# Kernel optimization log

Hardware: AMD Instinct MI355X
Metric: run time of the kernel (lower is better)

## Reference

```python
import jax, jax.numpy as jnp
import numpy as np

D_MODEL = 1024
B, T = 4, 2048
LN_EPS = 1e-5


def setup_inputs() -> dict:
    key = jax.random.key(0)
    ks = jax.random.split(key, 8)
    d = D_MODEL
    x = jax.random.normal(ks[0], (B, T, d), dtype=jnp.float32)
    # linear params (fan-in scaled)
    W_in = jax.random.normal(ks[1], (d, 4 * d), dtype=jnp.float32) / np.sqrt(d)
    b_in = jnp.zeros((4 * d,), dtype=jnp.float32)
    W_out = jax.random.normal(ks[2], (2 * d, d), dtype=jnp.float32) / np.sqrt(2 * d)
    b_out = jnp.zeros((d,), dtype=jnp.float32)
    # LRU initializer (matches the torch module's initializer())
    rng = np.random.default_rng(0)
    r_min, r_max = 0.9, 0.999
    u1 = rng.random(d)
    u2 = rng.random(d)
    nu_log = np.log(-0.5 * np.log(u1 * (r_max ** 2 - r_min ** 2) + r_min ** 2))
    theta_log = np.log(u2 * np.pi * 2)
    gamma_log = np.log(np.sqrt(1 - np.exp(-np.exp(nu_log)) ** 2))
    # LayerNorm affine params
    ln_w = jnp.ones((2 * d,), dtype=jnp.float32)
    ln_b = jnp.zeros((2 * d,), dtype=jnp.float32)
    return {
        "x": x,
        "W_in": W_in, "b_in": b_in,
        "nu_log": jnp.asarray(nu_log, dtype=jnp.float32),
        "theta_log": jnp.asarray(theta_log, dtype=jnp.float32),
        "gamma_log": jnp.asarray(gamma_log, dtype=jnp.float32),
        "ln_w": ln_w, "ln_b": ln_b,
        "W_out": W_out, "b_out": b_out,
    }


def _complex_scan(in_r, in_i, f_r, f_i):
    """h_t = f * h_{t-1} + in_t over axis=1, complex math in real/imag pairs."""
    def combine(l, r):
        a1r, a1i, b1r, b1i = l
        a2r, a2i, b2r, b2i = r
        ar = a2r * a1r - a2i * a1i
        ai = a2r * a1i + a2i * a1r
        br = a2r * b1r - a2i * b1i + b2r
        bi = a2r * b1i + a2i * b1r + b2i
        return (ar, ai, br, bi)
    fr = jnp.broadcast_to(f_r, in_r.shape)
    fi = jnp.broadcast_to(f_i, in_i.shape)
    _, _, hr, hi = jax.lax.associative_scan(combine, (fr, fi, in_r, in_i), axis=1)
    return hr, hi


def reference(x, W_in, b_in, nu_log, theta_log, gamma_log, ln_w, ln_b, W_out, b_out):
    d = x.shape[-1]
    u = x @ W_in + b_in                       # [B, T, 4d]
    v, o = u[..., :2 * d], u[..., 2 * d:]     # each [B, T, 2d]
    nu = jnp.exp(-jnp.exp(nu_log))            # [d]
    theta = jnp.exp(theta_log)
    gamma = jnpp_exp = jnp.exp(gamma_log)
    f_r = nu * jnp.cos(theta)
    f_i = nu * jnp.sin(theta)
    in_r = gamma * v[..., :d]                 # [B, T, d]
    in_i = gamma * v[..., d:]
    h_r, h_i = _complex_scan(in_r, in_i, f_r, f_i)
    y = jnp.concatenate([h_r, h_i], axis=-1) * jax.nn.silu(o)  # [B, T, 2d]
    mu = jnp.mean(y, axis=-1, keepdims=True)
    var = jnp.mean(jnp.square(y - mu), axis=-1, keepdims=True)
    y = (y - mu) * jax.lax.rsqrt(var + LN_EPS) * ln_w + ln_b
    return y @ W_out + b_out                  # [B, T, d]
```

## Files before the change

### kernel.cpp

```cpp
#include <hip/hip_runtime.h>
#include <hip/hip_bf16.h>

#define D_MODEL 1024
#define BB 4
#define TT 2048
#define ROWS (BB*TT)
#define NCHUNK 32
#define CHLEN 64

typedef __attribute__((ext_vector_type(8))) short short8;
typedef __attribute__((ext_vector_type(4))) float floatx4;

static __device__ __forceinline__ ushort f2bf(float f) {
    union { float f; unsigned u; } v; v.f = f;
    unsigned r = v.u + 0x7FFF + ((v.u >> 16) & 1);
    return (ushort)(r >> 16);
}
static __device__ __forceinline__ float bf2f(ushort b) {
    union { unsigned u; float f; } v; v.u = ((unsigned)b) << 16;
    return v.f;
}

#define GLOAD_LDS16(gp, lp)                                                 \
    __builtin_amdgcn_global_load_lds(                                       \
        (const __attribute__((address_space(1))) void*)(gp),                \
        (__attribute__((address_space(3))) void*)(lp), 16, 0, 0)

#define PREP_A 8192
#define PREP_B 4096
#define PREP_C 2048
__global__ __launch_bounds__(256) void prep_all(
    const float* __restrict__ x, ushort* __restrict__ xb,
    const float* __restrict__ W_in, ushort* __restrict__ WinT,
    const float* __restrict__ W_out, ushort* __restrict__ W1T,
    const float* __restrict__ lnw, const float* __restrict__ lnb,
    float* __restrict__ s1, float* __restrict__ c2,
    const float* __restrict__ nu_log, const float* __restrict__ theta_log,
    const float* __restrict__ gamma_log,
    float* __restrict__ fr, float* __restrict__ fi, float* __restrict__ gm) {
    __shared__ float smem[32 * 33 + 8 * 32 * 2];
    int bid = blockIdx.x, tid = threadIdx.x;
    if (bid < PREP_A) {
        int i = bid * 256 + tid;
        float4 v = ((const float4*)x)[i];
        ushort4 o;
        o.x = f2bf(v.x); o.y = f2bf(v.y); o.z = f2bf(v.z); o.w = f2bf(v.w);
        ((ushort4*)xb)[i] = o;
    } else if (bid < PREP_A + PREP_B) {
        int b2 = bid - PREP_A;
        int n0 = (b2 & 127) * 32, k0 = (b2 >> 7) * 32;
        int tx = tid & 31, ty = tid >> 5;
        float (*tile)[33] = (float (*)[33])smem;
#pragma unroll
        for (int j = 0; j < 4; ++j)
            tile[ty + j*8][tx] = W_in[(size_t)(k0 + ty + j*8) * 4096 + n0 + tx];
        __syncthreads();
#pragma unroll
        for (int j = 0; j < 4; ++j)
            WinT[(size_t)(n0 + ty + j*8) * 1024 + k0 + tx] = f2bf(tile[tx][ty + j*8]);
    } else if (bid < PREP_A + PREP_B + PREP_C) {
        int b2 = bid - PREP_A - PREP_B;
        int n0 = (b2 & 31) * 32, k0 = (b2 >> 5) * 32;
        int tx = tid & 31, ty = tid >> 5;
        float (*tile)[33] = (float (*)[33])smem;
        float* red1 = smem + 32 * 33;
        float* red2 = red1 + 8 * 32;
        float p1 = 0.f, p2 = 0.f;
#pragma unroll
        for (int j = 0; j < 4; ++j) {
            int k = k0 + ty + j * 8;
            float w = W_out[(size_t)k * 1024 + n0 + tx];
            float lw = lnw[k], lb = lnb[k];
            tile[ty + j*8][tx] = lw * w;
            p1 += lw * w; p2 += lb * w;
        }
        __syncthreads();
#pragma unroll
        for (int j = 0; j < 4; ++j)
            W1T[(size_t)(n0 + ty + j*8) * 2048 + k0 + tx] = f2bf(tile[tx][ty + j*8]);
        red1[ty * 32 + tx] = p1; red2[ty * 32 + tx] = p2;
        __syncthreads();
        if (ty == 0) {
            float a = 0.f, b = 0.f;
#pragma unroll
            for (int t = 0; t < 8; ++t) { a += red1[t * 32 + tx]; b += red2[t * 32 + tx]; }
            atomicAdd(&s1[n0 + tx], a);
            atomicAdd(&c2[n0 + tx], b);
        }
    } else {
        int c = (bid - PREP_A - PREP_B - PREP_C) * 256 + tid;
        if (c < D_MODEL) {
            float nu = expf(-expf(nu_log[c]));
            float th = expf(theta_log[c]);
            fr[c] = nu * cosf(th);
            fi[c] = nu * sinf(th);
            gm[c] = expf(gamma_log[c]);
        }
    }
}

#define P_PRE  do { __builtin_amdgcn_sched_barrier(0); __builtin_amdgcn_s_barrier();  \
                    asm volatile("s_waitcnt lgkmcnt(0)" ::: "memory");                \
                    __builtin_amdgcn_sched_barrier(0);                                \
                    __builtin_amdgcn_s_setprio(1); } while (0)
#define P_POST do { __builtin_amdgcn_s_setprio(0); __builtin_amdgcn_sched_barrier(0); \
                    __builtin_amdgcn_s_barrier();                                     \
                    __builtin_amdgcn_sched_barrier(0); } while (0)

__global__ __launch_bounds__(512) void gemm256(
    const ushort* __restrict__ A, const ushort* __restrict__ B,
    int K, int N, const float* __restrict__ bias, int mode,
    const float* __restrict__ gamma,
    ushort* __restrict__ out_r, ushort* __restrict__ out_i,
    ushort* __restrict__ out_o, float* __restrict__ outC,
    const float* __restrict__ mu, const float* __restrict__ rs,
    const float* __restrict__ s1, const float* __restrict__ c2) {
    __shared__ ushort LA[2][256 * 64];
    __shared__ ushort LB[2][256 * 64];
    int tid = threadIdx.x;
    int lane = tid & 63;
    int wave = tid >> 6;
    int wp = wave >> 2;
    int wq = wave & 3;
    int lr = lane & 15, q = lane >> 4;
    int swl = lr & 7;
    int rs8 = tid >> 3, ch = tid & 7;
    int sw8 = (ch ^ (rs8 & 7)) * 8;
    long m0 = (long)blockIdx.y * 256;
    long n0 = (long)blockIdx.x * 256;
    const int NT = K >> 6;

    const ushort* Abase = A + (size_t)(m0 + rs8) * K + sw8;
    const ushort* Bbase = B + (size_t)(n0 + rs8) * K + sw8;

    floatx4 acc[8][4] = {};

#define STG_A(kt, P, R) GLOAD_LDS16(Abase + (size_t)(R) * K + (kt), \
                                    &LA[P][((R) + rs8) * 64 + ch * 8])
#define STG_B(kt, P, R) GLOAD_LDS16(Bbase + (size_t)(R) * K + (kt), \
                                    &LB[P][((R) + rs8) * 64 + ch * 8])

    STG_A(0, 0, 0);    STG_A(0, 0, 64);
    STG_B(0, 0, 0);    STG_B(0, 0, 64);
    STG_B(0, 0, 128);  STG_B(0, 0, 192);
    STG_A(0, 0, 128);  STG_A(0, 0, 192);
    STG_A(64, 1, 0);   STG_A(64, 1, 64);
    STG_B(64, 1, 0);   STG_B(64, 1, 64);
    STG_B(64, 1, 128); STG_B(64, 1, 192);
    asm volatile("s_waitcnt vmcnt(6)" ::: "memory");
    __builtin_amdgcn_s_barrier();

    for (int t = 0; t < NT; ++t) {
        const int p = t & 1;
        int kt1 = (t + 1 < NT) ? (t + 1) << 6 : 0;
        int kt2 = (t + 2 < NT) ? (t + 2) << 6 : 0;
        short8 a[2][4], b0[2][2], b1[2][2];

#pragma unroll
        for (int ks = 0; ks < 2; ++ks) {
#pragma unroll
            for (int r = 0; r < 4; ++r)
                a[ks][r] = *(const short8*)&LA[p][(wp * 64 + r * 16 + lr) * 64 + ((ks * 4 + q) ^ swl) * 8];
#pragma unroll
            for (int c = 0; c < 2; ++c)
                b0[ks][c] = *(const short8*)&LB[p][(wq * 32 + c * 16 + lr) * 64 + ((ks * 4 + q) ^ swl) * 8];
        }
        STG_A(kt1, p ^ 1, 128); STG_A(kt1, p ^ 1, 192);
        P_PRE;
#pragma unroll
        for (int ks = 0; ks < 2; ++ks)
#pragma unroll
            for (int r = 0; r < 4; ++r)
#pragma unroll
                for (int c = 0; c < 2; ++c)
                    acc[r][c] = __builtin_amdgcn_mfma_f32_16x16x32_bf16(
                        a[ks][r], b0[ks][c], acc[r][c], 0, 0, 0);
        P_POST;

#pragma unroll
        for (int ks = 0; ks < 2; ++ks)
#pragma unroll
            for (int c = 0; c < 2; ++c)
                b1[ks][c] = *(const short8*)&LB[p][(128 + wq * 32 + c * 16 + lr) * 64 + ((ks * 4 + q) ^ swl) * 8];
        STG_A(kt2, p, 0); STG_A(kt2, p, 64);
        P_PRE;
#pragma unroll
        for (int ks = 0; ks < 2; ++ks)
#pragma unroll
            for (int r = 0; r < 4; ++r)
#pragma unroll
                for (int c = 0; c < 2; ++c)
                    acc[r][2 + c] = __builtin_amdgcn_mfma_f32_16x16x32_bf16(
                        a[ks][r], b1[ks][c], acc[r][2 + c], 0, 0, 0);
        P_POST;

#pragma unroll
        for (int ks = 0; ks < 2; ++ks)
#pragma unroll
            for (int r = 0; r < 4; ++r)
                a[ks][r] = *(const short8*)&LA[p][(128 + wp * 64 + r * 16 + lr) * 64 + ((ks * 4 + q) ^ swl) * 8];
        STG_B(kt2, p, 0); STG_B(kt2, p, 64);
        P_PRE;
#pragma unroll
        for (int ks = 0; ks < 2; ++ks)
#pragma unroll
            for (int r = 0; r < 4; ++r)
#pragma unroll
                for (int c = 0; c < 2; ++c)
                    acc[4 + r][c] = __builtin_amdgcn_mfma_f32_16x16x32_bf16(
                        a[ks][r], b0[ks][c], acc[4 + r][c], 0, 0, 0);
        P_POST;

        STG_B(kt2, p, 128); STG_B(kt2, p, 192);
        asm volatile("s_waitcnt vmcnt(6)" ::: "memory");
        P_PRE;
#pragma unroll
        for (int ks = 0; ks < 2; ++ks)
#pragma unroll
            for (int r = 0; r < 4; ++r)
#pragma unroll
                for (int c = 0; c < 2; ++c)
                    acc[4 + r][2 + c] = __builtin_amdgcn_mfma_f32_16x16x32_bf16(
                        a[ks][r], b1[ks][c], acc[4 + r][2 + c], 0, 0, 0);
        P_POST;
    }
    asm volatile("s_waitcnt vmcnt(0)" ::: "memory");

    if (mode == 2) {
#pragma unroll
        for (int nh = 0; nh < 2; ++nh)
#pragma unroll
            for (int c = 0; c < 2; ++c) {
                long col = n0 + nh * 128 + wq * 32 + c * 16 + lr;
                float bc = c2[col] + bias[col];
                float s1c = s1[col];
#pragma unroll
                for (int mh = 0; mh < 2; ++mh)
#pragma unroll
                    for (int r = 0; r < 4; ++r)
#pragma unroll
                        for (int g = 0; g < 4; ++g) {
                            long row = m0 + mh * 128 + wp * 64 + r * 16 + q * 4 + g;
                            outC[row * (long)N + col] =
                                rs[row] * (acc[mh * 4 + r][nh * 2 + c][g] - mu[row] * s1c) + bc;
                        }
            }
    } else {
        int sector = (int)(n0 >> 10);
        if (sector < 2) {
            ushort* dst = sector ? out_i : out_r;
#pragma unroll
            for (int nh = 0; nh < 2; ++nh)
#pragma unroll
                for (int c = 0; c < 2; ++c) {
                    int lc = (int)(n0 & 1023) + nh * 128 + wq * 32 + c * 16 + lr;
                    float bv = bias[(sector << 10) + lc];
                    float gv = gamma[lc];
#pragma unroll
                    for (int mh = 0; mh < 2; ++mh)
#pragma unroll
                        for (int r = 0; r < 4; ++r)
#pragma unroll
                            for (int g = 0; g < 4; ++g) {
                                long row = m0 + mh * 128 + wp * 64 + r * 16 + q * 4 + g;
                                dst[row * 1024 + lc] = f2bf(gv * (acc[mh * 4 + r][nh * 2 + c][g] + bv));
                            }
                }
        } else {
            int oc0 = (int)(n0 - 2048);
#pragma unroll
            for (int nh = 0; nh < 2; ++nh)
#pragma unroll
                for (int c = 0; c < 2; ++c) {
                    int oc = oc0 + nh * 128 + wq * 32 + c * 16 + lr;
                    float bv = bias[2048 + oc];
#pragma unroll
                    for (int mh = 0; mh < 2; ++mh)
#pragma unroll
                        for (int r = 0; r < 4; ++r)
#pragma unroll
                            for (int g = 0; g < 4; ++g) {
                                long row = m0 + mh * 128 + wp * 64 + r * 16 + q * 4 + g;
                                out_o[row * 2048 + oc] = f2bf(acc[mh * 4 + r][nh * 2 + c][g] + bv);
                            }
                }
        }
    }
#undef STG_A
#undef STG_B
}

__global__ __launch_bounds__(256) void scan_carries(
    const ushort* __restrict__ in_r, const ushort* __restrict__ in_i,
    float* __restrict__ carry,
    const float* __restrict__ fr_, const float* __restrict__ fi_) {
    int t = blockIdx.x * 256 + threadIdx.x;
    int c = t & 1023;
    int ck = (t >> 10) & (NCHUNK - 1);
    int b = t >> 15;
    float fr = fr_[c], fi = fi_[c];
    size_t base = ((size_t)(b * TT + ck * CHLEN)) * 1024 + c;
    float hr = 0.f, hi = 0.f;
#pragma unroll 4
    for (int j = 0; j < CHLEN; ++j) {
        size_t idx = base + (size_t)j * 1024;
        float r = bf2f(in_r[idx]), im = bf2f(in_i[idx]);
        float nhr = fr * hr - fi * hi + r;
        float nhi = fr * hi + fi * hr + im;
        hr = nhr; hi = nhi;
    }
    size_t ci = (((size_t)b * 1024 + c) * NCHUNK + ck) * 2;
    carry[ci] = hr; carry[ci + 1] = hi;
}

__global__ __launch_bounds__(256) void scan_apply(
    const ushort* __restrict__ in_r, const ushort* __restrict__ in_i,
    const float* __restrict__ carry,
    const float* __restrict__ fr_, const float* __restrict__ fi_,
    const ushort* __restrict__ o, ushort* __restrict__ yb) {
    int t = blockIdx.x * 256 + threadIdx.x;
    int c = t & 1023;
    int ck = (t >> 10) & (NCHUNK - 1);
    int b = t >> 15;
    float fr = fr_[c], fi = fi_[c];
    float ar = fr, ai = fi;
#pragma unroll
    for (int s = 0; s < 6; ++s) {
        float nr = ar * ar - ai * ai, ni = 2.f * ar * ai;
        ar = nr; ai = ni;
    }
    float Hr = 0.f, Hi = 0.f;
    size_t cb = ((size_t)b * 1024 + c) * NCHUNK * 2;
    for (int k = 0; k < ck; ++k) {
        float cr = carry[cb + k * 2], cim = carry[cb + k * 2 + 1];
        float nHr = ar * Hr - ai * Hi + cr;
        float nHi = ar * Hi + ai * Hr + cim;
        Hr = nHr; Hi = nHi;
    }
    size_t base = ((size_t)(b * TT + ck * CHLEN)) * 1024 + c;
    size_t rowbase = (size_t)(b * TT + ck * CHLEN);
    float hr = Hr, hi = Hi;
#pragma unroll 2
    for (int j = 0; j < CHLEN; ++j) {
        size_t idx = base + (size_t)j * 1024;
        float r = bf2f(in_r[idx]), im = bf2f(in_i[idx]);
        float nhr = fr * hr - fi * hi + r;
        float nhi = fr * hi + fi * hr + im;
        hr = nhr; hi = nhi;
        size_t ob = (rowbase + j) * 2048 + c;
        float ov1 = bf2f(o[ob]);
        float ov2 = bf2f(o[ob + 1024]);
        float y1 = hr * ov1 / (1.f + __expf(-ov1));
        float y2 = hi * ov2 / (1.f + __expf(-ov2));
        yb[ob] = f2bf(y1);
        yb[ob + 1024] = f2bf(y2);
    }
}

__global__ __launch_bounds__(256) void row_stats(
    const ushort* __restrict__ yb, float* __restrict__ mu_o,
    float* __restrict__ rs_o) {
    long row = blockIdx.x;
    int tid = threadIdx.x;
    const ushort* p = yb + row * 2048 + tid * 8;
    uint4 raw = *(const uint4*)p;
    float s = 0.f, s2 = 0.f;
    unsigned w[4] = {raw.x, raw.y, raw.z, raw.w};
#pragma unroll
    for (int j = 0; j < 4; ++j) {
        float a = bf2f((ushort)(w[j] & 0xffff));
        float b = bf2f((ushort)(w[j] >> 16));
        s += a + b; s2 += a * a + b * b;
    }
#pragma unroll
    for (int off = 32; off > 0; off >>= 1) {
        s += __shfl_down(s, off, 64);
        s2 += __shfl_down(s2, off, 64);
    }
    __shared__ float red[8];
    int wv = tid >> 6;
    if ((tid & 63) == 0) { red[wv] = s; red[4 + wv] = s2; }
    __syncthreads();
    if (tid == 0) {
        s = red[0] + red[1] + red[2] + red[3];
        s2 = red[4] + red[5] + red[6] + red[7];
        float mu = s * (1.f / 2048.f);
        float var = s2 * (1.f / 2048.f) - mu * mu;
        mu_o[row] = mu;
        rs_o[row] = rsqrtf(var + 1e-5f);
    }
}


extern "C" void kernel_launch(void* const* d_in, const int* in_sizes, int n_in,
                              void* d_out, int out_size, void* d_ws, size_t ws_size,
                              hipStream_t stream) {
    const float* x         = (const float*)d_in[0];
    const float* W_in      = (const float*)d_in[1];
    const float* b_in      = (const float*)d_in[2];
    const float* nu_log    = (const float*)d_in[3];
    const float* theta_log = (const float*)d_in[4];
    const float* gamma_log = (const float*)d_in[5];
    const float* ln_w      = (const float*)d_in[6];
    const float* ln_b      = (const float*)d_in[7];
    const float* W_out     = (const float*)d_in[8];
    const float* b_out     = (const float*)d_in[9];
    float* out = (float*)d_out;

    char* ws = (char*)d_ws;
    size_t off = 0;
    auto alloc = [&](size_t bytes) {
        char* p = ws + off;
        off += (bytes + 255) & ~(size_t)255;
        return p;
    };
    ushort* xb    = (ushort*)alloc((size_t)ROWS * 1024 * 2);
    ushort* WinT  = (ushort*)alloc((size_t)4096 * 1024 * 2);
    ushort* W1T   = (ushort*)alloc((size_t)1024 * 2048 * 2);
    float*  fr    = (float*)alloc(1024 * 4);
    float*  fi    = (float*)alloc(1024 * 4);
    float*  gm    = (float*)alloc(1024 * 4);
    float*  s1c2  = (float*)alloc(2048 * 4);
    float*  s1    = s1c2;
    float*  c2    = s1c2 + 1024;
    ushort* in_r  = (ushort*)alloc((size_t)ROWS * 1024 * 2);
    ushort* in_i  = (ushort*)alloc((size_t)ROWS * 1024 * 2);
    ushort* obuf  = (ushort*)alloc((size_t)ROWS * 2048 * 2);
    float*  carry = (float*)alloc((size_t)BB * 1024 * NCHUNK * 2 * 4);
    ushort* yb    = (ushort*)alloc((size_t)ROWS * 2048 * 2);
    float*  muv   = (float*)alloc(ROWS * 4);
    float*  rsv   = (float*)alloc(ROWS * 4);

    hipMemsetAsync(s1c2, 0, 2048 * 4, stream);

    prep_all<<<PREP_A + PREP_B + PREP_C + 4, 256, 0, stream>>>(
        x, xb, W_in, WinT, W_out, W1T, ln_w, ln_b, s1, c2,
        nu_log, theta_log, gamma_log, fr, fi, gm);

    gemm256<<<dim3(4096 / 256, ROWS / 256), 512, 0, stream>>>(
        xb, WinT, 1024, 4096, b_in, 1, gm, in_r, in_i, obuf, nullptr,
        nullptr, nullptr, nullptr, nullptr);

    scan_carries<<<BB * 1024 * NCHUNK / 256, 256, 0, stream>>>(in_r, in_i, carry, fr, fi);
    scan_apply<<<BB * 1024 * NCHUNK / 256, 256, 0, stream>>>(
        in_r, in_i, carry, fr, fi, obuf, yb);

    row_stats<<<ROWS, 256, 0, stream>>>(yb, muv, rsv);

    gemm256<<<dim3(1024 / 256, ROWS / 256), 512, 0, stream>>>(
        yb, W1T, 2048, 1024, b_out, 2, nullptr, nullptr, nullptr, nullptr, out,
        muv, rsv, s1, c2);
}
```

Measured before the change: 315.2 us.

## Split GEMM kernels, remap workgroups, vectorize scan and add carry prefix kernel

Specializes the 256-tile GEMM to the input projection only, and adds a workgroup-id remap that spreads consecutive blocks across 8 groups, presumably to spread them across XCDs. The output projection moves to a new 128x128 tile GEMM with single-buffered LDS, so the 1024-wide output gets 512 workgroups instead of 128. The scan kernels now process two channels per thread with 32-bit vector loads and stores. The per-chunk serial carry recomputation in scan_apply is replaced by a separate carry_prefix kernel that runs the prefix once. Costs include an extra launch, a carry_prefix grid of only 8 blocks, and a simpler non-pipelined GEMM for the output projection.

```diff
diff --git a/kernel.cpp b/kernel.cpp
--- a/kernel.cpp
+++ b/kernel.cpp
@@ -109,12 +109,10 @@
 
 __global__ __launch_bounds__(512) void gemm256(
     const ushort* __restrict__ A, const ushort* __restrict__ B,
-    int K, int N, const float* __restrict__ bias, int mode,
+    int K, const float* __restrict__ bias,
     const float* __restrict__ gamma,
     ushort* __restrict__ out_r, ushort* __restrict__ out_i,
-    ushort* __restrict__ out_o, float* __restrict__ outC,
-    const float* __restrict__ mu, const float* __restrict__ rs,
-    const float* __restrict__ s1, const float* __restrict__ c2) {
+    ushort* __restrict__ out_o) {
     __shared__ ushort LA[2][256 * 64];
     __shared__ ushort LB[2][256 * 64];
     int tid = threadIdx.x;
@@ -126,8 +124,14 @@
     int swl = lr & 7;
     int rs8 = tid >> 3, ch = tid & 7;
     int sw8 = (ch ^ (rs8 & 7)) * 8;
-    long m0 = (long)blockIdx.y * 256;
-    long n0 = (long)blockIdx.x * 256;
+
+    int gx = gridDim.x;
+    int nwg = gx * gridDim.y;
+    int lid = blockIdx.y * gx + blockIdx.x;
+    int per = nwg >> 3;
+    int sid = (lid & 7) * per + (lid >> 3);
+    long m0 = (long)(sid / gx) * 256;
+    long n0 = (long)(sid % gx) * 256;
     const int NT = K >> 6;
 
     const ushort* Abase = A + (size_t)(m0 + rs8) * K + sw8;
@@ -226,14 +230,16 @@
     }
     asm volatile("s_waitcnt vmcnt(0)" ::: "memory");
 
-    if (mode == 2) {
+    int sector = (int)(n0 >> 10);
+    if (sector < 2) {
+        ushort* dst = sector ? out_i : out_r;
 #pragma unroll
         for (int nh = 0; nh < 2; ++nh)
 #pragma unroll
             for (int c = 0; c < 2; ++c) {
-                long col = n0 + nh * 128 + wq * 32 + c * 16 + lr;
-                float bc = c2[col] + bias[col];
-                float s1c = s1[col];
+                int lc = (int)(n0 & 1023) + nh * 128 + wq * 32 + c * 16 + lr;
+                float bv = bias[(sector << 10) + lc];
+                float gv = gamma[lc];
 #pragma unroll
                 for (int mh = 0; mh < 2; ++mh)
 #pragma unroll
@@ -241,53 +247,100 @@
 #pragma unroll
                         for (int g = 0; g < 4; ++g) {
                             long row = m0 + mh * 128 + wp * 64 + r * 16 + q * 4 + g;
-                            outC[row * (long)N + col] =
-                                rs[row] * (acc[mh * 4 + r][nh * 2 + c][g] - mu[row] * s1c) + bc;
+                            dst[row * 1024 + lc] = f2bf(gv * (acc[mh * 4 + r][nh * 2 + c][g] + bv));
                         }
             }
     } else {
-        int sector = (int)(n0 >> 10);
-        if (sector < 2) {
-            ushort* dst = sector ? out_i : out_r;
-#pragma unroll
-            for (int nh = 0; nh < 2; ++nh)
-#pragma unroll
-                for (int c = 0; c < 2; ++c) {
-                    int lc = (int)(n0 & 1023) + nh * 128 + wq * 32 + c * 16 + lr;
-                    float bv = bias[(sector << 10) + lc];
-                    float gv = gamma[lc];
-#pragma unroll
-                    for (int mh = 0; mh < 2; ++mh)
-#pragma unroll
-                        for (int r = 0; r < 4; ++r)
-#pragma unroll
-                            for (int g = 0; g < 4; ++g) {
-                                long row = m0 + mh * 128 + wp * 64 + r * 16 + q * 4 + g;
-                                dst[row * 1024 + lc] = f2bf(gv * (acc[mh * 4 + r][nh * 2 + c][g] + bv));
-                            }
-                }
-        } else {
-            int oc0 = (int)(n0 - 2048);
-#pragma unroll
-            for (int nh = 0; nh < 2; ++nh)
-#pragma unroll
-                for (int c = 0; c < 2; ++c) {
-                    int oc = oc0 + nh * 128 + wq * 32 + c * 16 + lr;
-                    float bv = bias[2048 + oc];
-#pragma unroll
-                    for (int mh = 0; mh < 2; ++mh)
-#pragma unroll
-                        for (int r = 0; r < 4; ++r)
-#pragma unroll
-                            for (int g = 0; g < 4; ++g) {
-                                long row = m0 + mh * 128 + wp * 64 + r * 16 + q * 4 + g;
-                                out_o[row * 2048 + oc] = f2bf(acc[mh * 4 + r][nh * 2 + c][g] + bv);
-                            }
-                }
-        }
+        int oc0 = (int)(n0 - 2048);
+#pragma unroll
+        for (int nh = 0; nh < 2; ++nh)
+#pragma unroll
+            for (int c = 0; c < 2; ++c) {
+                int oc = oc0 + nh * 128 + wq * 32 + c * 16 + lr;
+                float bv = bias[2048 + oc];
+#pragma unroll
+                for (int mh = 0; mh < 2; ++mh)
+#pragma unroll
+                    for (int r = 0; r < 4; ++r)
+#pragma unroll
+                        for (int g = 0; g < 4; ++g) {
+                            long row = m0 + mh * 128 + wp * 64 + r * 16 + q * 4 + g;
+                            out_o[row * 2048 + oc] = f2bf(acc[mh * 4 + r][nh * 2 + c][g] + bv);
+                        }
+            }
     }
 #undef STG_A
 #undef STG_B
+}
+
+__global__ __launch_bounds__(256) void gemm128(
+    const ushort* __restrict__ A, const ushort* __restrict__ B,
+    int K, int N, const float* __restrict__ bias, float* __restrict__ outC,
+    const float* __restrict__ mu, const float* __restrict__ rs,
+    const float* __restrict__ s1, const float* __restrict__ c2) {
+    __shared__ ushort As[128 * 64];
+    __shared__ ushort Bs[128 * 64];
+    int tid = threadIdx.x;
+    int lane = tid & 63, wave = tid >> 6;
+    int wm = (wave & 1) * 64, wn = (wave >> 1) * 64;
+    int lr = lane & 15, q = lane >> 4;
+    int gx = gridDim.x;
+    int nwg = gx * gridDim.y;
+    int lid = blockIdx.y * gx + blockIdx.x;
+    int per = nwg >> 3;
+    int sid = (lid & 7) * per + (lid >> 3);
+    long m0 = (long)(sid / gx) * 128;
+    long n0 = (long)(sid % gx) * 128;
+    floatx4 acc[4][4] = {};
+
+    int rs_ = tid >> 3;
+    int pg = ((tid & 7) ^ (rs_ & 7)) * 8;
+    const ushort* Ap = A + (m0 + rs_) * (long)K + pg;
+    const ushort* Bp = B + (n0 + rs_) * (long)K + pg;
+    int swl = lr & 7;
+
+    for (int kt = 0; kt < K; kt += 64) {
+        __syncthreads();
+#pragma unroll
+        for (int j = 0; j < 4; ++j) {
+            GLOAD_LDS16(Ap + kt + (long)(j * 32) * K, &As[(j * 256 + tid) * 8]);
+            GLOAD_LDS16(Bp + kt + (long)(j * 32) * K, &Bs[(j * 256 + tid) * 8]);
+        }
+        __syncthreads();
+#pragma unroll
+        for (int s = 0; s < 2; ++s) {
+            short8 af[4], bfv[4];
+            int pq = ((s * 4 + q) ^ swl) * 8;
+#pragma unroll
+            for (int r = 0; r < 4; ++r)
+                af[r] = *(const short8*)&As[(wm + r * 16 + lr) * 64 + pq];
+#pragma unroll
+            for (int c = 0; c < 4; ++c)
+                bfv[c] = *(const short8*)&Bs[(wn + c * 16 + lr) * 64 + pq];
+#pragma unroll
+            for (int r = 0; r < 4; ++r)
+#pragma unroll
+                for (int c = 0; c < 4; ++c)
+                    acc[r][c] = __builtin_amdgcn_mfma_f32_16x16x32_bf16(
+                        af[r], bfv[c], acc[r][c], 0, 0, 0);
+        }
+    }
+
+#pragma unroll
+    for (int r = 0; r < 4; ++r) {
+#pragma unroll
+        for (int c = 0; c < 4; ++c) {
+            long col = n0 + wn + c * 16 + lr;
+            float bc = c2[col] + bias[col];
+            float s1c = s1[col];
+#pragma unroll
+            for (int g = 0; g < 4; ++g) {
+                long row = m0 + wm + r * 16 + q * 4 + g;
+                outC[row * (long)N + col] =
+                    rs[row] * (acc[r][c][g] - mu[row] * s1c) + bc;
+            }
+        }
+    }
 }
 
 __global__ __launch_bounds__(256) void scan_carries(
@@ -295,22 +348,53 @@
     float* __restrict__ carry,
     const float* __restrict__ fr_, const float* __restrict__ fi_) {
     int t = blockIdx.x * 256 + threadIdx.x;
-    int c = t & 1023;
-    int ck = (t >> 10) & (NCHUNK - 1);
-    int b = t >> 15;
-    float fr = fr_[c], fi = fi_[c];
-    size_t base = ((size_t)(b * TT + ck * CHLEN)) * 1024 + c;
-    float hr = 0.f, hi = 0.f;
-#pragma unroll 4
+    int cp = t & 511;
+    int ck = (t >> 9) & (NCHUNK - 1);
+    int b = t >> 14;
+    int c0 = cp * 2;
+    float f0r = fr_[c0], f0i = fi_[c0], f1r = fr_[c0 + 1], f1i = fi_[c0 + 1];
+    size_t base = ((size_t)(b * TT + ck * CHLEN)) * 1024 + c0;
+    float h0r = 0.f, h0i = 0.f, h1r = 0.f, h1i = 0.f;
+#pragma unroll 8
     for (int j = 0; j < CHLEN; ++j) {
-        size_t idx = base + (size_t)j * 1024;
-        float r = bf2f(in_r[idx]), im = bf2f(in_i[idx]);
-        float nhr = fr * hr - fi * hi + r;
-        float nhi = fr * hi + fi * hr + im;
-        hr = nhr; hi = nhi;
-    }
-    size_t ci = (((size_t)b * 1024 + c) * NCHUNK + ck) * 2;
-    carry[ci] = hr; carry[ci + 1] = hi;
+        uint ur = *(const uint*)(in_r + base + (size_t)j * 1024);
+        uint ui = *(const uint*)(in_i + base + (size_t)j * 1024);
+        float r0 = bf2f((ushort)ur), r1 = bf2f((ushort)(ur >> 16));
+        float i0 = bf2f((ushort)ui), i1 = bf2f((ushort)(ui >> 16));
+        float n0r = f0r * h0r - f0i * h0i + r0;
+        float n0i = f0r * h0i + f0i * h0r + i0;
+        float n1r = f1r * h1r - f1i * h1i + r1;
+        float n1i = f1r * h1i + f1i * h1r + i1;
+        h0r = n0r; h0i = n0i; h1r = n1r; h1i = n1i;
+    }
+    ((float4*)carry)[((size_t)b * NCHUNK + ck) * 512 + cp] =
+        make_float4(h0r, h0i, h1r, h1i);
+}
+
+__global__ __launch_bounds__(256) void carry_prefix(
+    float* __restrict__ carry,
+    const float* __restrict__ fr_, const float* __restrict__ fi_) {
+    int t = blockIdx.x * 256 + threadIdx.x;
+    int cp = t & 511, b = t >> 9;
+    int c0 = cp * 2;
+    float a0r = fr_[c0], a0i = fi_[c0], a1r = fr_[c0 + 1], a1i = fi_[c0 + 1];
+#pragma unroll
+    for (int s = 0; s < 6; ++s) {
+        float t0r = a0r * a0r - a0i * a0i, t0i = 2.f * a0r * a0i;
+        float t1r = a1r * a1r - a1i * a1i, t1i = 2.f * a1r * a1i;
+        a0r = t0r; a0i = t0i; a1r = t1r; a1i = t1i;
+    }
+    float4* base = (float4*)carry + (size_t)b * NCHUNK * 512 + cp;
+    float C0r = 0.f, C0i = 0.f, C1r = 0.f, C1i = 0.f;
+    for (int k = 0; k < NCHUNK; ++k) {
+        float4 s = base[(size_t)k * 512];
+        base[(size_t)k * 512] = make_float4(C0r, C0i, C1r, C1i);
+        float n0r = a0r * C0r - a0i * C0i + s.x;
+        float n0i = a0r * C0i + a0i * C0r + s.y;
+        float n1r = a1r * C1r - a1i * C1i + s.z;
+        float n1i = a1r * C1i + a1i * C1r + s.w;
+        C0r = n0r; C0i = n0i; C1r = n1r; C1i = n1i;
+    }
 }
 
 __global__ __launch_bounds__(256) void scan_apply(
@@ -319,41 +403,37 @@
     const float* __restrict__ fr_, const float* __restrict__ fi_,
     const ushort* __restrict__ o, ushort* __restrict__ yb) {
     int t = blockIdx.x * 256 + threadIdx.x;
-    int c = t & 1023;
-    int ck = (t >> 10) & (NCHUNK - 1);
-    int b = t >> 15;
-    float fr = fr_[c], fi = fi_[c];
-    float ar = fr, ai = fi;
-#pragma unroll
-    for (int s = 0; s < 6; ++s) {
-        float nr = ar * ar - ai * ai, ni = 2.f * ar * ai;
-        ar = nr; ai = ni;
-    }
-    float Hr = 0.f, Hi = 0.f;
-    size_t cb = ((size_t)b * 1024 + c) * NCHUNK * 2;
-    for (int k = 0; k < ck; ++k) {
-        float cr = carry[cb + k * 2], cim = carry[cb + k * 2 + 1];
-        float nHr = ar * Hr - ai * Hi + cr;
-        float nHi = ar * Hi + ai * Hr + cim;
-        Hr = nHr; Hi = nHi;
-    }
-    size_t base = ((size_t)(b * TT + ck * CHLEN)) * 1024 + c;
+    int cp = t & 511;
+    int ck = (t >> 9) & (NCHUNK - 1);
+    int b = t >> 14;
+    int c0 = cp * 2;
+    float f0r = fr_[c0], f0i = fi_[c0], f1r = fr_[c0 + 1], f1i = fi_[c0 + 1];
+    float4 C = ((const float4*)carry)[((size_t)b * NCHUNK + ck) * 512 + cp];
+    float h0r = C.x, h0i = C.y, h1r = C.z, h1i = C.w;
+    size_t base = ((size_t)(b * TT + ck * CHLEN)) * 1024 + c0;
     size_t rowbase = (size_t)(b * TT + ck * CHLEN);
-    float hr = Hr, hi = Hi;
-#pragma unroll 2
+#pragma unroll 4
     for (int j = 0; j < CHLEN; ++j) {
-        size_t idx = base + (size_t)j * 1024;
-        float r = bf2f(in_r[idx]), im = bf2f(in_i[idx]);
-        float nhr = fr * hr - fi * hi + r;
-        float nhi = fr * hi + fi * hr + im;
-        hr = nhr; hi = nhi;
-        size_t ob = (rowbase + j) * 2048 + c;
-        float ov1 = bf2f(o[ob]);
-        float ov2 = bf2f(o[ob + 1024]);
-        float y1 = hr * ov1 / (1.f + __expf(-ov1));
-        float y2 = hi * ov2 / (1.f + __expf(-ov2));
-        yb[ob] = f2bf(y1);
-        yb[ob + 1024] = f2bf(y2);
+        uint ur = *(const uint*)(in_r + base + (size_t)j * 1024);
+        uint ui = *(const uint*)(in_i + base + (size_t)j * 1024);
+        size_t ob = (rowbase + j) * 2048 + c0;
+        uint uo1 = *(const uint*)(o + ob);
+        uint uo2 = *(const uint*)(o + ob + 1024);
+        float r0 = bf2f((ushort)ur), r1 = bf2f((ushort)(ur >> 16));
+        float i0 = bf2f((ushort)ui), i1 = bf2f((ushort)(ui >> 16));
+        float n0r = f0r * h0r - f0i * h0i + r0;
+        float n0i = f0r * h0i + f0i * h0r + i0;
+        float n1r = f1r * h1r - f1i * h1i + r1;
+        float n1i = f1r * h1i + f1i * h1r + i1;
+        h0r = n0r; h0i = n0i; h1r = n1r; h1i = n1i;
+        float o00 = bf2f((ushort)uo1), o01 = bf2f((ushort)(uo1 >> 16));
+        float o10 = bf2f((ushort)uo2), o11 = bf2f((ushort)(uo2 >> 16));
+        float y00 = h0r * o00 / (1.f + __expf(-o00));
+        float y01 = h1r * o01 / (1.f + __expf(-o01));
+        float y10 = h0i * o10 / (1.f + __expf(-o10));
+        float y11 = h1i * o11 / (1.f + __expf(-o11));
+        *(uint*)(yb + ob) = (uint)f2bf(y00) | ((uint)f2bf(y01) << 16);
+        *(uint*)(yb + ob + 1024) = (uint)f2bf(y10) | ((uint)f2bf(y11) << 16);
     }
 }
 
@@ -438,16 +518,15 @@
         nu_log, theta_log, gamma_log, fr, fi, gm);
 
     gemm256<<<dim3(4096 / 256, ROWS / 256), 512, 0, stream>>>(
-        xb, WinT, 1024, 4096, b_in, 1, gm, in_r, in_i, obuf, nullptr,
-        nullptr, nullptr, nullptr, nullptr);
-
-    scan_carries<<<BB * 1024 * NCHUNK / 256, 256, 0, stream>>>(in_r, in_i, carry, fr, fi);
-    scan_apply<<<BB * 1024 * NCHUNK / 256, 256, 0, stream>>>(
+        xb, WinT, 1024, b_in, gm, in_r, in_i, obuf);
+
+    scan_carries<<<BB * 512 * NCHUNK / 256, 256, 0, stream>>>(in_r, in_i, carry, fr, fi);
+    carry_prefix<<<BB * 512 / 256, 256, 0, stream>>>(carry, fr, fi);
+    scan_apply<<<BB * 512 * NCHUNK / 256, 256, 0, stream>>>(
         in_r, in_i, carry, fr, fi, obuf, yb);
 
     row_stats<<<ROWS, 256, 0, stream>>>(yb, muv, rsv);
 
-    gemm256<<<dim3(1024 / 256, ROWS / 256), 512, 0, stream>>>(
-        yb, W1T, 2048, 1024, b_out, 2, nullptr, nullptr, nullptr, nullptr, out,
-        muv, rsv, s1, c2);
-}
+    gemm128<<<dim3(1024 / 128, ROWS / 128), 256, 0, stream>>>(
+        yb, W1T, 2048, 1024, b_out, out, muv, rsv, s1, c2);
+}
```

Measured after the change: 275.8 us. 12.5% less time.
